# Performance work log

Measured on AMD Instinct MI355X. Metric: run time of the kernel, lower is better.

The kernel has to match this reference:

```python
import jax, jax.numpy as jnp
import numpy as np

EPS = 1e-6
BASE_CURVATURE = 1.0


def _artanh(x):
    return jnp.arctanh(jnp.clip(x, -1.0 + 1e-5, 1.0 - 1e-5))


def _norm(x):
    return jnp.maximum(jnp.linalg.norm(x, axis=-1, keepdims=True), EPS)


def _logmap0(x, c):
    # Poincare-ball log map at origin
    sc = jnp.sqrt(c)
    n = _norm(x)
    return _artanh(sc * n) * x / (sc * n)


def _expmap0(v, c):
    # Poincare-ball exp map at origin
    sc = jnp.sqrt(c)
    n = _norm(v)
    return jnp.tanh(sc * n) * v / (sc * n)


def _mobius_add(x, y, c):
    x2 = jnp.sum(x * x, axis=-1, keepdims=True)
    y2 = jnp.sum(y * y, axis=-1, keepdims=True)
    xy = jnp.sum(x * y, axis=-1, keepdims=True)
    num = (1.0 + 2.0 * c * xy + c * y2) * x + (1.0 - c * x2) * y
    den = 1.0 + 2.0 * c * xy + (c * c) * x2 * y2
    return num / jnp.maximum(den, EPS)


def _mobius_scalar_mul(t, x, c):
    sc = jnp.sqrt(c)
    n = _norm(x)
    return jnp.tanh(t * _artanh(sc * n)) * x / (sc * n)


def setup_inputs() -> dict:
    key = jax.random.key(0)
    ks = jax.random.split(key, 8)
    B, D_in, D_out, K = 4096, 2048, 2048, 4
    scale_w = np.sqrt(2.0 / (D_in + D_out)) * 0.1
    return {
        "x": jax.random.normal(ks[0], (B, D_in), jnp.float32) * 0.05,
        "weight": jax.random.normal(ks[1], (D_out, D_in), jnp.float32) * scale_w,
        "bias": jax.random.normal(ks[2], (D_out,), jnp.float32) * 0.01,
        "curv_weight": jax.random.normal(ks[3], (1, D_in), jnp.float32) * 0.1,
        "curv_bias": jnp.zeros((1,), jnp.float32),
        "anchors": jax.random.normal(ks[4], (K, D_out), jnp.float32) * 0.3,
        "t_values": jnp.full((K,), 0.5, jnp.float32),
        "anchor_weights": jnp.full((K,), 1.0 / K, jnp.float32),
    }


def reference(x, weight, bias, curv_weight, curv_bias, anchors, t_values, anchor_weights):
    # 1) dynamic curvature prediction: c_i = base_c * softplus(x . w + b), then mean
    logits = x @ curv_weight[0] + curv_bias[0]                 # [B]
    curvatures = BASE_CURVATURE * jax.nn.softplus(logits)      # [B]
    c = jax.lax.stop_gradient(jnp.mean(curvatures))            # scalar (.item() in torch)

    # 2) fused hyperbolic linear: expmap0(logmap0(x) @ W^T + b)
    u = _logmap0(x, c)                                         # [B, D_in]
    h = u @ weight.T + bias                                    # [B, D_out]
    y = _expmap0(h, c)                                         # [B, D_out]

    # 3) geodesic activation: weighted Mobius geodesic toward each anchor
    xe = y[:, None, :]                                         # [B, 1, D]
    a = anchors[None, :, :]                                    # [1, K, D]
    diff = _mobius_add(-xe, a, c)                              # [B, K, D]
    step = _mobius_scalar_mul(t_values[None, :, None], diff, c)
    g = _mobius_add(xe, step, c)                               # [B, K, D]
    w = jax.nn.softmax(anchor_weights)                         # [K]
    return jnp.einsum("bkd,k->bd", g, w)                       # [B, D_out]
```

## Files before the change

kernel.cpp:

```cpp
#include <hip/hip_runtime.h>
#include <stdint.h>

#define B_ROWS 4096
#define D_IN   2048
#define D_OUT  2048
#define KANCH  4

typedef _Float16 half8  __attribute__((ext_vector_type(8)));
typedef _Float16 half4  __attribute__((ext_vector_type(4)));
typedef float    floatx4 __attribute__((ext_vector_type(4)));
typedef const __attribute__((address_space(1))) uint8_t* gptr_t;
typedef __attribute__((address_space(3))) uint8_t* lptr_t;

__device__ __forceinline__ float frcp(float x)   { return __builtin_amdgcn_rcpf(x); }
__device__ __forceinline__ float ftanh(float x)  { float e = __expf(2.f * x); return (e - 1.f) * frcp(e + 1.f); }
__device__ __forceinline__ float fatanh(float z) { return 0.5f * __logf((1.f + z) * frcp(1.f - z)); }

__global__ __launch_bounds__(256) void k_prep(
    const float* __restrict__ x,
    const float* __restrict__ W,
    const float* __restrict__ cw,
    const float* __restrict__ cb,
    const float* __restrict__ bias,
    const float* __restrict__ anchors,
    _Float16* __restrict__ xh,
    _Float16* __restrict__ Wh,
    float* __restrict__ n2x,
    float* __restrict__ spart,
    float* __restrict__ scal)
{
    int tid = threadIdx.x;
    if (blockIdx.x < 1024) {
        int w = tid >> 6, lane = tid & 63;
        int row = blockIdx.x * 4 + w;
        const floatx4* xr = (const floatx4*)(x + (size_t)row * D_IN);
        const floatx4* wr = (const floatx4*)cw;
        _Float16* xo = xh + (size_t)row * D_IN;
        float dot = 0.f, ss = 0.f;
#pragma unroll
        for (int i = 0; i < 8; ++i) {
            int idx = i * 64 + lane;
            floatx4 xv = xr[idx];
            floatx4 wv = wr[idx];
#pragma unroll
            for (int j = 0; j < 4; ++j) {
                dot += xv[j] * wv[j];
                ss  += xv[j] * xv[j];
            }
            half4 h = {(_Float16)xv[0], (_Float16)xv[1], (_Float16)xv[2], (_Float16)xv[3]};
            *(half4*)(xo + idx * 4) = h;
        }
#pragma unroll
        for (int off = 32; off; off >>= 1) {
            dot += __shfl_down(dot, off);
            ss  += __shfl_down(ss, off);
        }
        __shared__ float spw[4];
        if (lane == 0) {
            n2x[row] = ss;
            float z = dot + cb[0];
            spw[w] = (z > 20.f) ? z : log1pf(expf(z));
        }
        __syncthreads();
        if (tid == 0)
            spart[blockIdx.x] = spw[0] + spw[1] + spw[2] + spw[3];
    } else if (blockIdx.x < 2048) {
        int blk = blockIdx.x - 1024;
        const floatx4* W4 = (const floatx4*)W;
#pragma unroll
        for (int i = 0; i < 4; ++i) {
            int idx = blk * 1024 + i * 256 + tid;
            floatx4 v = W4[idx];
            half4 h = {(_Float16)v[0], (_Float16)v[1], (_Float16)v[2], (_Float16)v[3]};
            *(half4*)(Wh + (size_t)idx * 4) = h;
        }
    } else {
        int w = tid >> 6, lane = tid & 63;
        float bf[8], af[KANCH][8];
        *(floatx4*)(bf)     = *(const floatx4*)(bias + tid * 8);
        *(floatx4*)(bf + 4) = *(const floatx4*)(bias + tid * 8 + 4);
#pragma unroll
        for (int k = 0; k < KANCH; ++k) {
            *(floatx4*)(af[k])     = *(const floatx4*)(anchors + (size_t)k * D_OUT + tid * 8);
            *(floatx4*)(af[k] + 4) = *(const floatx4*)(anchors + (size_t)k * D_OUT + tid * 8 + 4);
        }
        float v[9];
#pragma unroll
        for (int q = 0; q < 9; ++q) v[q] = 0.f;
#pragma unroll
        for (int j = 0; j < 8; ++j) {
            v[0] += bf[j] * bf[j];
#pragma unroll
            for (int k = 0; k < KANCH; ++k) {
                v[1 + k] += bf[j] * af[k][j];
                v[5 + k] += af[k][j] * af[k][j];
            }
        }
#pragma unroll
        for (int off = 32; off; off >>= 1)
#pragma unroll
            for (int q = 0; q < 9; ++q) v[q] += __shfl_down(v[q], off);
        __shared__ float red[4][9];
        if (lane == 0)
#pragma unroll
            for (int q = 0; q < 9; ++q) red[w][q] = v[q];
        __syncthreads();
        if (tid == 0)
#pragma unroll
            for (int q = 0; q < 9; ++q)
                scal[1 + q] = red[0][q] + red[1][q] + red[2][q] + red[3][q];
    }
}

template<int KPB>
__global__ __launch_bounds__(512, 2) void k_gemm(
    const _Float16* __restrict__ A,
    const _Float16* __restrict__ W,
    _Float16* __restrict__ P0,
    _Float16* __restrict__ P1)
{
    constexpr int NT = KPB / 64;
    __shared__ __align__(16) _Float16 lds[2][2][2][8192];
    const int tid  = threadIdx.x;
    const int lane = tid & 63;
    const int w    = tid >> 6;
    const int wm   = w >> 2;
    const int wn   = w & 3;
    const int bm0  = blockIdx.y * 256;
    const int bn0  = blockIdx.x * 256;
    const int kbase = blockIdx.z * KPB;
    _Float16* P = (blockIdx.z == 0) ? P0 : P1;

    const int e0 = tid * 16;
    const int srow = w * 16 + (lane & 15);
    const int scol = (lane >> 4) * 8;
    const size_t asrc = (size_t)(bm0 + srow) * D_IN + scol + kbase;
    const size_t bsrc = (size_t)(bn0 + srow) * D_IN + scol + kbase;
    const int wmoff = wm * 8192;
    const int wnoff = wn * 4096;
    const int loff  = lane * 16;

#define STAGE_Q(OP, D, KH, GP, SRC, KB) do { \
    uint8_t* qb_ = (uint8_t*)&lds[OP][D][KH][0]; \
    __builtin_amdgcn_global_load_lds((gptr_t)((GP) + (SRC) + (KB)), (lptr_t)(qb_ + e0), 16, 0, 0); \
    __builtin_amdgcn_global_load_lds((gptr_t)((GP) + (SRC) + (size_t)128 * D_IN + (KB)), (lptr_t)(qb_ + e0 + 8192), 16, 0, 0); \
} while (0)

    floatx4 acc[8][4];
#pragma unroll
    for (int mi = 0; mi < 8; ++mi)
#pragma unroll
        for (int ni = 0; ni < 4; ++ni)
            acc[mi][ni] = (floatx4){0.f, 0.f, 0.f, 0.f};

    STAGE_Q(0, 0, 0, A, asrc, 0);
    STAGE_Q(0, 0, 1, A, asrc, 32);
    STAGE_Q(1, 0, 0, W, bsrc, 0);
    STAGE_Q(1, 0, 1, W, bsrc, 32);
    STAGE_Q(0, 1, 0, A, asrc, 64);
    STAGE_Q(1, 1, 0, W, bsrc, 64);
    STAGE_Q(1, 1, 1, W, bsrc, 96);
    asm volatile("s_waitcnt vmcnt(6)" ::: "memory");
    __builtin_amdgcn_s_barrier();
    __builtin_amdgcn_sched_barrier(0);

    half8 aq[4], bq[4];

#define LOAD_A4(D, KH, MI0) do { _Pragma("unroll") \
    for (int mi = 0; mi < 4; ++mi) \
        aq[mi] = *(const half8*)((const uint8_t*)&lds[0][D][KH][0] + wmoff + ((MI0) + mi) * 1024 + loff); \
} while (0)
#define LOAD_B4(D, KH) do { _Pragma("unroll") \
    for (int ni = 0; ni < 4; ++ni) \
        bq[ni] = *(const half8*)((const uint8_t*)&lds[1][D][KH][0] + wnoff + ni * 1024 + loff); \
} while (0)
#define MFMA16(MI0) do { \
    __builtin_amdgcn_s_barrier(); \
    asm volatile("s_waitcnt lgkmcnt(0)" ::: "memory"); \
    __builtin_amdgcn_sched_barrier(0); \
    __builtin_amdgcn_s_setprio(1); \
    _Pragma("unroll") for (int mi = 0; mi < 4; ++mi) \
    _Pragma("unroll") for (int ni = 0; ni < 4; ++ni) \
        acc[(MI0) + mi][ni] = __builtin_amdgcn_mfma_f32_16x16x32_f16(aq[mi], bq[ni], acc[(MI0) + mi][ni], 0, 0, 0); \
    __builtin_amdgcn_s_setprio(0); \
    __builtin_amdgcn_sched_barrier(0); \
} while (0)
#define ENDPH() do { __builtin_amdgcn_s_barrier(); __builtin_amdgcn_sched_barrier(0); } while (0)

#define TILE_BODY(T, D) do { \
    LOAD_A4(D, 0, 0); LOAD_B4(D, 0); \
    if ((T) + 1 < NT) STAGE_Q(0, (D) ^ 1, 1, A, asrc, ((T) + 1) * 64 + 32); \
    MFMA16(0); ENDPH(); \
    LOAD_A4(D, 0, 4); \
    if ((T) + 2 < NT) STAGE_Q(1, D, 0, W, bsrc, ((T) + 2) * 64); \
    MFMA16(4); ENDPH(); \
    LOAD_A4(D, 1, 0); LOAD_B4(D, 1); \
    if ((T) + 2 < NT) STAGE_Q(0, D, 0, A, asrc, ((T) + 2) * 64); \
    MFMA16(0); ENDPH(); \
    LOAD_A4(D, 1, 4); \
    if ((T) + 2 < NT) STAGE_Q(1, D, 1, W, bsrc, ((T) + 2) * 64 + 32); \
    MFMA16(4); \
    if ((T) < NT - 2) asm volatile("s_waitcnt vmcnt(6)" ::: "memory"); \
    else              asm volatile("s_waitcnt vmcnt(0)" ::: "memory"); \
    ENDPH(); \
} while (0)

    for (int t = 0; t < NT; t += 2) {
        TILE_BODY(t, 0);
        TILE_BODY(t + 1, 1);
    }

#undef TILE_BODY
#undef ENDPH
#undef MFMA16
#undef LOAD_B4
#undef LOAD_A4
#undef STAGE_Q

#pragma unroll
    for (int mi = 0; mi < 8; ++mi) {
#pragma unroll
        for (int r = 0; r < 4; ++r) {
            int gm = bm0 + wm * 128 + mi * 16 + (lane >> 4) * 4 + r;
#pragma unroll
            for (int ni = 0; ni < 4; ++ni) {
                int gn = bn0 + wn * 64 + ni * 16 + (lane & 15);
                P[(size_t)gm * D_OUT + gn] = (_Float16)acc[mi][ni][r];
            }
        }
    }
}

__global__ __launch_bounds__(256) void k_mobius(
    const _Float16* __restrict__ P0,
    const _Float16* __restrict__ P1,
    const float* __restrict__ bias,
    const float* __restrict__ anchors,
    const float* __restrict__ tv,
    const float* __restrict__ aw,
    const float* __restrict__ n2x,
    const float* __restrict__ spart,
    const float* __restrict__ scal,
    int split,
    float* __restrict__ out)
{
    int tid = threadIdx.x, w = tid >> 6, lane = tid & 63;
    size_t rowoff = (size_t)blockIdx.x * D_OUT;
    float pf[8], bf[8];
    {
        half8 p = *(const half8*)(P0 + rowoff + tid * 8);
#pragma unroll
        for (int j = 0; j < 8; ++j) pf[j] = (float)p[j];
    }
    if (split == 2) {
        half8 q = *(const half8*)(P1 + rowoff + tid * 8);
#pragma unroll
        for (int j = 0; j < 8; ++j) pf[j] += (float)q[j];
    }
    *(floatx4*)(bf)     = *(const floatx4*)(bias + tid * 8);
    *(floatx4*)(bf + 4) = *(const floatx4*)(bias + tid * 8 + 4);
    float af[KANCH][8];
#pragma unroll
    for (int k = 0; k < KANCH; ++k) {
        *(floatx4*)(af[k])     = *(const floatx4*)(anchors + (size_t)k * D_OUT + tid * 8);
        *(floatx4*)(af[k] + 4) = *(const floatx4*)(anchors + (size_t)k * D_OUT + tid * 8 + 4);
    }
    float v[7];
#pragma unroll
    for (int q = 0; q < 7; ++q) v[q] = 0.f;
    {
        floatx4 s4 = ((const floatx4*)spart)[tid];
        v[6] = s4[0] + s4[1] + s4[2] + s4[3];
    }
#pragma unroll
    for (int j = 0; j < 8; ++j) {
        v[0] += pf[j] * pf[j];
        v[1] += pf[j] * bf[j];
#pragma unroll
        for (int k = 0; k < KANCH; ++k) v[2 + k] += pf[j] * af[k][j];
    }
#pragma unroll
    for (int off = 32; off; off >>= 1)
#pragma unroll
        for (int q = 0; q < 7; ++q) v[q] += __shfl_down(v[q], off);
    __shared__ float red[4][7];
    __shared__ float cf[2 + KANCH];
    if (lane == 0)
#pragma unroll
        for (int q = 0; q < 7; ++q) red[w][q] = v[q];
    __syncthreads();
    if (w == 0) {
        int k = lane & 3;
        float pp = red[0][0] + red[1][0] + red[2][0] + red[3][0];
        float pb = red[0][1] + red[1][1] + red[2][1] + red[3][1];
        float pa = red[0][2 + k] + red[1][2 + k] + red[2][2 + k] + red[3][2 + k];
        float spsum = red[0][6] + red[1][6] + red[2][6] + red[3][6];
        float bb = scal[1];
        float ba = scal[2 + k];
        float aa = scal[6 + k];
        float c = spsum * (1.0f / (float)B_ROWS);
        float sc = __builtin_amdgcn_sqrtf(c);
        float nx = fmaxf(__builtin_amdgcn_sqrtf(n2x[blockIdx.x]), 1e-6f);
        float ax = sc * nx;
        float zx = fminf(fmaxf(ax, -1.f + 1e-5f), 1.f - 1e-5f);
        float f = fatanh(zx) * frcp(ax);
        float hh = f * f * pp + 2.f * f * pb + bb;
        float ha = f * pa + ba;
        float ek = __expf(aw[k]);
        float se = ek;
        se += __shfl_xor(se, 1);
        se += __shfl_xor(se, 2);
        float wk = ek * frcp(se);
        float nh = fmaxf(__builtin_amdgcn_sqrtf(hh), 1e-6f);
        float snh = sc * nh;
        float gy = ftanh(snh) * frcp(snh);
        float x2 = gy * gy * hh;
        float B1 = 1.f - c * x2;
        float y2 = aa;
        float dy = gy * ha;
        float A1 = 1.f - 2.f * c * dy + c * y2;
        float den1 = fmaxf(1.f - 2.f * c * dy + c * c * x2 * y2, 1e-6f);
        float rd1 = frcp(den1);
        float al = -A1 * rd1, be = B1 * rd1;
        float nd2 = fmaxf(al * al * x2 + 2.f * al * be * dy + be * be * y2, 0.f);
        float nd = fmaxf(__builtin_amdgcn_sqrtf(nd2), 1e-6f);
        float snd = sc * nd;
        float zc = fminf(fmaxf(snd, -1.f + 1e-5f), 1.f - 1e-5f);
        float s = ftanh(tv[k] * fatanh(zc)) * frcp(snd);
        float y2s = s * s * nd2;
        float xys = s * (al * x2 + be * dy);
        float A2 = 1.f + 2.f * c * xys + c * y2s;
        float den2 = fmaxf(1.f + 2.f * c * xys + c * c * x2 * y2s, 1e-6f);
        float rd2 = frcp(den2);
        float Cy  = (A2 + B1 * s * al) * rd2;
        float Cak = (B1 * s * be) * rd2;
        float chk = wk * Cy;
        chk += __shfl_xor(chk, 1);
        chk += __shfl_xor(chk, 2);
        if (lane == 0) {
            float c0 = gy * chk;
            cf[0] = c0 * f;
            cf[1] = c0;
        }
        if (lane < 4) cf[2 + lane] = wk * Cak;
    }
    __syncthreads();
    float cp = cf[0], cb_ = cf[1];
    float o[8];
#pragma unroll
    for (int j = 0; j < 8; ++j) {
        float val = cp * pf[j] + cb_ * bf[j];
#pragma unroll
        for (int k = 0; k < KANCH; ++k) val += cf[2 + k] * af[k][j];
        o[j] = val;
    }
    *(floatx4*)(out + rowoff + tid * 8)     = *(floatx4*)(o);
    *(floatx4*)(out + rowoff + tid * 8 + 4) = *(floatx4*)(o + 4);
}

extern "C" void kernel_launch(void* const* d_in, const int* in_sizes, int n_in,
                              void* d_out, int out_size, void* d_ws, size_t ws_size,
                              hipStream_t stream) {
    const float* x       = (const float*)d_in[0];
    const float* wt      = (const float*)d_in[1];
    const float* bias    = (const float*)d_in[2];
    const float* cw      = (const float*)d_in[3];
    const float* cb      = (const float*)d_in[4];
    const float* anchors = (const float*)d_in[5];
    const float* tv      = (const float*)d_in[6];
    const float* aw      = (const float*)d_in[7];
    float* out = (float*)d_out;

    _Float16* Wh = (_Float16*)d_ws;
    _Float16* xh = Wh + (size_t)D_OUT * D_IN;
    float* n2x   = (float*)(xh + (size_t)B_ROWS * D_IN);
    float* spart = n2x + B_ROWS;
    float* scal  = spart + 1024;
    _Float16* P0 = (_Float16*)(scal + 16);
    _Float16* P1 = P0 + (size_t)B_ROWS * D_OUT;
    size_t need2 = (size_t)((char*)(P1 + (size_t)B_ROWS * D_OUT) - (char*)d_ws);
    int split = (ws_size >= need2) ? 2 : 1;

    k_prep<<<2049, 256, 0, stream>>>(x, wt, cw, cb, bias, anchors, xh, Wh, n2x, spart, scal);
    if (split == 2)
        k_gemm<D_IN / 2><<<dim3(D_OUT / 256, B_ROWS / 256, 2), 512, 0, stream>>>(xh, Wh, P0, P1);
    else
        k_gemm<D_IN><<<dim3(D_OUT / 256, B_ROWS / 256, 1), 512, 0, stream>>>(xh, Wh, P0, P1);
    k_mobius<<<B_ROWS, 256, 0, stream>>>(P0, P1, bias, anchors, tv, aw, n2x, spart, scal, split, out);
}
```

Measured before the change: 162.3 us.

## Remap GEMM tiles per XCD, relax sched barriers, batch rows in mobius

The GEMM block index is remapped so each of the 8 XCDs works on a compact group of M/N tiles (and a single K-split half), which should improve L2 reuse of A and W inside each XCD. The sched_barrier and explicit lgkmcnt waits around the MFMA phases are removed, so the compiler handles LDS-load/MFMA ordering. The mobius kernel now processes 8 rows per block, loading bias/anchors and computing curvature/softmax once per block instead of once per row. Removing the explicit waits leaves synchronization of LDS reads to the compiler's inserted waitcnts, and fewer mobius blocks lowers parallelism.

```diff
diff --git a/kernel.cpp b/kernel.cpp
--- a/kernel.cpp
+++ b/kernel.cpp
@@ -5,6 +5,7 @@
 #define D_IN   2048
 #define D_OUT  2048
 #define KANCH  4
+#define MROWS  8
 
 typedef _Float16 half8  __attribute__((ext_vector_type(8)));
 typedef _Float16 half4  __attribute__((ext_vector_type(4)));
@@ -120,16 +121,32 @@
     _Float16* __restrict__ P1)
 {
     constexpr int NT = KPB / 64;
+    constexpr int NZ = (KPB == D_IN) ? 1 : 2;
     __shared__ __align__(16) _Float16 lds[2][2][2][8192];
     const int tid  = threadIdx.x;
     const int lane = tid & 63;
     const int w    = tid >> 6;
     const int wm   = w >> 2;
     const int wn   = w & 3;
-    const int bm0  = blockIdx.y * 256;
-    const int bn0  = blockIdx.x * 256;
-    const int kbase = blockIdx.z * KPB;
-    _Float16* P = (blockIdx.z == 0) ? P0 : P1;
+
+    int lin = (blockIdx.z * gridDim.y + blockIdx.y) * gridDim.x + blockIdx.x;
+    int xcd = lin & 7;
+    int i   = lin >> 3;
+    int zz, mt, nt;
+    if (NZ == 2) {
+        zz = xcd & 1;
+        int grp = xcd >> 1;
+        mt = (grp >> 1) * 8 + (i >> 2);
+        nt = (grp & 1) * 4 + (i & 3);
+    } else {
+        zz = 0;
+        mt = (xcd >> 1) * 4 + (i >> 2);
+        nt = (xcd & 1) * 4 + (i & 3);
+    }
+    const int bm0 = mt * 256;
+    const int bn0 = nt * 256;
+    const int kbase = zz * KPB;
+    _Float16* P = (zz == 0) ? P0 : P1;
 
     const int e0 = tid * 16;
     const int srow = w * 16 + (lane & 15);
@@ -162,7 +179,6 @@
     STAGE_Q(1, 1, 1, W, bsrc, 96);
     asm volatile("s_waitcnt vmcnt(6)" ::: "memory");
     __builtin_amdgcn_s_barrier();
-    __builtin_amdgcn_sched_barrier(0);
 
     half8 aq[4], bq[4];
 
@@ -176,16 +192,13 @@
 } while (0)
 #define MFMA16(MI0) do { \
     __builtin_amdgcn_s_barrier(); \
-    asm volatile("s_waitcnt lgkmcnt(0)" ::: "memory"); \
-    __builtin_amdgcn_sched_barrier(0); \
     __builtin_amdgcn_s_setprio(1); \
     _Pragma("unroll") for (int mi = 0; mi < 4; ++mi) \
     _Pragma("unroll") for (int ni = 0; ni < 4; ++ni) \
         acc[(MI0) + mi][ni] = __builtin_amdgcn_mfma_f32_16x16x32_f16(aq[mi], bq[ni], acc[(MI0) + mi][ni], 0, 0, 0); \
     __builtin_amdgcn_s_setprio(0); \
-    __builtin_amdgcn_sched_barrier(0); \
 } while (0)
-#define ENDPH() do { __builtin_amdgcn_s_barrier(); __builtin_amdgcn_sched_barrier(0); } while (0)
+#define ENDPH() __builtin_amdgcn_s_barrier()
 
 #define TILE_BODY(T, D) do { \
     LOAD_A4(D, 0, 0); LOAD_B4(D, 0); \
@@ -245,18 +258,7 @@
     float* __restrict__ out)
 {
     int tid = threadIdx.x, w = tid >> 6, lane = tid & 63;
-    size_t rowoff = (size_t)blockIdx.x * D_OUT;
-    float pf[8], bf[8];
-    {
-        half8 p = *(const half8*)(P0 + rowoff + tid * 8);
-#pragma unroll
-        for (int j = 0; j < 8; ++j) pf[j] = (float)p[j];
-    }
-    if (split == 2) {
-        half8 q = *(const half8*)(P1 + rowoff + tid * 8);
-#pragma unroll
-        for (int j = 0; j < 8; ++j) pf[j] += (float)q[j];
-    }
+    float bf[8];
     *(floatx4*)(bf)     = *(const floatx4*)(bias + tid * 8);
     *(floatx4*)(bf + 4) = *(const floatx4*)(bias + tid * 8 + 4);
     float af[KANCH][8];
@@ -265,97 +267,124 @@
         *(floatx4*)(af[k])     = *(const floatx4*)(anchors + (size_t)k * D_OUT + tid * 8);
         *(floatx4*)(af[k] + 4) = *(const floatx4*)(anchors + (size_t)k * D_OUT + tid * 8 + 4);
     }
-    float v[7];
-#pragma unroll
-    for (int q = 0; q < 7; ++q) v[q] = 0.f;
+    float v6;
     {
         floatx4 s4 = ((const floatx4*)spart)[tid];
-        v[6] = s4[0] + s4[1] + s4[2] + s4[3];
-    }
-#pragma unroll
-    for (int j = 0; j < 8; ++j) {
-        v[0] += pf[j] * pf[j];
-        v[1] += pf[j] * bf[j];
-#pragma unroll
-        for (int k = 0; k < KANCH; ++k) v[2 + k] += pf[j] * af[k][j];
-    }
-#pragma unroll
-    for (int off = 32; off; off >>= 1)
-#pragma unroll
-        for (int q = 0; q < 7; ++q) v[q] += __shfl_down(v[q], off);
-    __shared__ float red[4][7];
+        v6 = s4[0] + s4[1] + s4[2] + s4[3];
+    }
+#pragma unroll
+    for (int off = 32; off; off >>= 1) v6 += __shfl_down(v6, off);
+    __shared__ float redS[4];
+    __shared__ float red[4][6];
     __shared__ float cf[2 + KANCH];
-    if (lane == 0)
-#pragma unroll
-        for (int q = 0; q < 7; ++q) red[w][q] = v[q];
+    if (lane == 0) redS[w] = v6;
     __syncthreads();
+
+    int k = lane & 3;
+    float c = 0.f, sc = 0.f, wk = 0.f, tvk = 0.f, bb = 0.f, ba = 0.f, aa = 0.f;
     if (w == 0) {
-        int k = lane & 3;
-        float pp = red[0][0] + red[1][0] + red[2][0] + red[3][0];
-        float pb = red[0][1] + red[1][1] + red[2][1] + red[3][1];
-        float pa = red[0][2 + k] + red[1][2 + k] + red[2][2 + k] + red[3][2 + k];
-        float spsum = red[0][6] + red[1][6] + red[2][6] + red[3][6];
-        float bb = scal[1];
-        float ba = scal[2 + k];
-        float aa = scal[6 + k];
-        float c = spsum * (1.0f / (float)B_ROWS);
-        float sc = __builtin_amdgcn_sqrtf(c);
-        float nx = fmaxf(__builtin_amdgcn_sqrtf(n2x[blockIdx.x]), 1e-6f);
-        float ax = sc * nx;
-        float zx = fminf(fmaxf(ax, -1.f + 1e-5f), 1.f - 1e-5f);
-        float f = fatanh(zx) * frcp(ax);
-        float hh = f * f * pp + 2.f * f * pb + bb;
-        float ha = f * pa + ba;
+        float spsum = redS[0] + redS[1] + redS[2] + redS[3];
+        c  = spsum * (1.0f / (float)B_ROWS);
+        sc = __builtin_amdgcn_sqrtf(c);
         float ek = __expf(aw[k]);
         float se = ek;
         se += __shfl_xor(se, 1);
         se += __shfl_xor(se, 2);
-        float wk = ek * frcp(se);
-        float nh = fmaxf(__builtin_amdgcn_sqrtf(hh), 1e-6f);
-        float snh = sc * nh;
-        float gy = ftanh(snh) * frcp(snh);
-        float x2 = gy * gy * hh;
-        float B1 = 1.f - c * x2;
-        float y2 = aa;
-        float dy = gy * ha;
-        float A1 = 1.f - 2.f * c * dy + c * y2;
-        float den1 = fmaxf(1.f - 2.f * c * dy + c * c * x2 * y2, 1e-6f);
-        float rd1 = frcp(den1);
-        float al = -A1 * rd1, be = B1 * rd1;
-        float nd2 = fmaxf(al * al * x2 + 2.f * al * be * dy + be * be * y2, 0.f);
-        float nd = fmaxf(__builtin_amdgcn_sqrtf(nd2), 1e-6f);
-        float snd = sc * nd;
-        float zc = fminf(fmaxf(snd, -1.f + 1e-5f), 1.f - 1e-5f);
-        float s = ftanh(tv[k] * fatanh(zc)) * frcp(snd);
-        float y2s = s * s * nd2;
-        float xys = s * (al * x2 + be * dy);
-        float A2 = 1.f + 2.f * c * xys + c * y2s;
-        float den2 = fmaxf(1.f + 2.f * c * xys + c * c * x2 * y2s, 1e-6f);
-        float rd2 = frcp(den2);
-        float Cy  = (A2 + B1 * s * al) * rd2;
-        float Cak = (B1 * s * be) * rd2;
-        float chk = wk * Cy;
-        chk += __shfl_xor(chk, 1);
-        chk += __shfl_xor(chk, 2);
-        if (lane == 0) {
-            float c0 = gy * chk;
-            cf[0] = c0 * f;
-            cf[1] = c0;
-        }
-        if (lane < 4) cf[2 + lane] = wk * Cak;
-    }
-    __syncthreads();
-    float cp = cf[0], cb_ = cf[1];
-    float o[8];
-#pragma unroll
-    for (int j = 0; j < 8; ++j) {
-        float val = cp * pf[j] + cb_ * bf[j];
-#pragma unroll
-        for (int k = 0; k < KANCH; ++k) val += cf[2 + k] * af[k][j];
-        o[j] = val;
-    }
-    *(floatx4*)(out + rowoff + tid * 8)     = *(floatx4*)(o);
-    *(floatx4*)(out + rowoff + tid * 8 + 4) = *(floatx4*)(o + 4);
+        wk = ek * frcp(se);
+        tvk = tv[k];
+        bb = scal[1];
+        ba = scal[2 + k];
+        aa = scal[6 + k];
+    }
+
+    for (int r = 0; r < MROWS; ++r) {
+        int row = blockIdx.x * MROWS + r;
+        size_t rowoff = (size_t)row * D_OUT;
+        float pf[8];
+        {
+            half8 p = *(const half8*)(P0 + rowoff + tid * 8);
+#pragma unroll
+            for (int j = 0; j < 8; ++j) pf[j] = (float)p[j];
+        }
+        if (split == 2) {
+            half8 q = *(const half8*)(P1 + rowoff + tid * 8);
+#pragma unroll
+            for (int j = 0; j < 8; ++j) pf[j] += (float)q[j];
+        }
+        float v[6];
+#pragma unroll
+        for (int q = 0; q < 6; ++q) v[q] = 0.f;
+#pragma unroll
+        for (int j = 0; j < 8; ++j) {
+            v[0] += pf[j] * pf[j];
+            v[1] += pf[j] * bf[j];
+#pragma unroll
+            for (int kk = 0; kk < KANCH; ++kk) v[2 + kk] += pf[j] * af[kk][j];
+        }
+#pragma unroll
+        for (int off = 32; off; off >>= 1)
+#pragma unroll
+            for (int q = 0; q < 6; ++q) v[q] += __shfl_down(v[q], off);
+        if (lane == 0)
+#pragma unroll
+            for (int q = 0; q < 6; ++q) red[w][q] = v[q];
+        __syncthreads();
+        if (w == 0) {
+            float pp = red[0][0] + red[1][0] + red[2][0] + red[3][0];
+            float pb = red[0][1] + red[1][1] + red[2][1] + red[3][1];
+            float pa = red[0][2 + k] + red[1][2 + k] + red[2][2 + k] + red[3][2 + k];
+            float nx = fmaxf(__builtin_amdgcn_sqrtf(n2x[row]), 1e-6f);
+            float ax = sc * nx;
+            float zx = fminf(fmaxf(ax, -1.f + 1e-5f), 1.f - 1e-5f);
+            float f = fatanh(zx) * frcp(ax);
+            float hh = f * f * pp + 2.f * f * pb + bb;
+            float ha = f * pa + ba;
+            float nh = fmaxf(__builtin_amdgcn_sqrtf(hh), 1e-6f);
+            float snh = sc * nh;
+            float gy = ftanh(snh) * frcp(snh);
+            float x2 = gy * gy * hh;
+            float B1 = 1.f - c * x2;
+            float y2 = aa;
+            float dy = gy * ha;
+            float A1 = 1.f - 2.f * c * dy + c * y2;
+            float den1 = fmaxf(1.f - 2.f * c * dy + c * c * x2 * y2, 1e-6f);
+            float rd1 = frcp(den1);
+            float al = -A1 * rd1, be = B1 * rd1;
+            float nd2 = fmaxf(al * al * x2 + 2.f * al * be * dy + be * be * y2, 0.f);
+            float nd = fmaxf(__builtin_amdgcn_sqrtf(nd2), 1e-6f);
+            float snd = sc * nd;
+            float zc = fminf(fmaxf(snd, -1.f + 1e-5f), 1.f - 1e-5f);
+            float s = ftanh(tvk * fatanh(zc)) * frcp(snd);
+            float y2s = s * s * nd2;
+            float xys = s * (al * x2 + be * dy);
+            float A2 = 1.f + 2.f * c * xys + c * y2s;
+            float den2 = fmaxf(1.f + 2.f * c * xys + c * c * x2 * y2s, 1e-6f);
+            float rd2 = frcp(den2);
+            float Cy  = (A2 + B1 * s * al) * rd2;
+            float Cak = (B1 * s * be) * rd2;
+            float chk = wk * Cy;
+            chk += __shfl_xor(chk, 1);
+            chk += __shfl_xor(chk, 2);
+            if (lane == 0) {
+                float c0 = gy * chk;
+                cf[0] = c0 * f;
+                cf[1] = c0;
+            }
+            if (lane < 4) cf[2 + lane] = wk * Cak;
+        }
+        __syncthreads();
+        float cp = cf[0], cb_ = cf[1];
+        float o[8];
+#pragma unroll
+        for (int j = 0; j < 8; ++j) {
+            float val = cp * pf[j] + cb_ * bf[j];
+#pragma unroll
+            for (int kk = 0; kk < KANCH; ++kk) val += cf[2 + kk] * af[kk][j];
+            o[j] = val;
+        }
+        *(floatx4*)(out + rowoff + tid * 8)     = *(floatx4*)(o);
+        *(floatx4*)(out + rowoff + tid * 8 + 4) = *(floatx4*)(o + 4);
+    }
 }
 
 extern "C" void kernel_launch(void* const* d_in, const int* in_sizes, int n_in,
@@ -383,8 +412,8 @@
 
     k_prep<<<2049, 256, 0, stream>>>(x, wt, cw, cb, bias, anchors, xh, Wh, n2x, spart, scal);
     if (split == 2)
-        k_gemm<D_IN / 2><<<dim3(D_OUT / 256, B_ROWS / 256, 2), 512, 0, stream>>>(xh, Wh, P0, P1);
+        k_gemm<D_IN / 2><<<dim3(8, 16, 2), 512, 0, stream>>>(xh, Wh, P0, P1);
     else
-        k_gemm<D_IN><<<dim3(D_OUT / 256, B_ROWS / 256, 1), 512, 0, stream>>>(xh, Wh, P0, P1);
-    k_mobius<<<B_ROWS, 256, 0, stream>>>(P0, P1, bias, anchors, tv, aw, n2x, spart, scal, split, out);
+        k_gemm<D_IN><<<dim3(8, 16, 1), 512, 0, stream>>>(xh, Wh, P0, P1);
+    k_mobius<<<B_ROWS / MROWS, 256, 0, stream>>>(P0, P1, bias, anchors, tv, aw, n2x, spart, scal, split, out);
 }
```

Result: slower. 168.6 us (+3.9%).

## Remap GEMM blocks per XCD and double-buffer LDS fragment loads across phases

Applied to the files above, without the earlier changes.

Replaces the hardware block order with an XCD-aware mapping, so blocks on the same XCD share M/N tiles and the K-split half, which should improve L2 reuse. Restructures the inner tile loop so the LDS fragment reads for the next MFMA phase are issued before the barrier and current phase's MFMAs. It uses separate even and odd register sets for this. The explicit lgkmcnt(0) waits and sched_barriers are dropped and the compiler now inserts the waits. This raises register pressure and relies on the barrier placement to avoid races between LDS reads and async global-to-LDS staging into the same buffers.

```diff
diff --git a/kernel.cpp b/kernel.cpp
--- a/kernel.cpp
+++ b/kernel.cpp
@@ -120,16 +120,32 @@
     _Float16* __restrict__ P1)
 {
     constexpr int NT = KPB / 64;
+    constexpr int NZ = (KPB == D_IN) ? 1 : 2;
     __shared__ __align__(16) _Float16 lds[2][2][2][8192];
     const int tid  = threadIdx.x;
     const int lane = tid & 63;
     const int w    = tid >> 6;
     const int wm   = w >> 2;
     const int wn   = w & 3;
-    const int bm0  = blockIdx.y * 256;
-    const int bn0  = blockIdx.x * 256;
-    const int kbase = blockIdx.z * KPB;
-    _Float16* P = (blockIdx.z == 0) ? P0 : P1;
+
+    int lin = (blockIdx.z * gridDim.y + blockIdx.y) * gridDim.x + blockIdx.x;
+    int xcd = lin & 7;
+    int i   = lin >> 3;
+    int zz, mt, nt;
+    if (NZ == 2) {
+        zz = xcd & 1;
+        int grp = xcd >> 1;
+        mt = (grp >> 1) * 8 + (i >> 2);
+        nt = (grp & 1) * 4 + (i & 3);
+    } else {
+        zz = 0;
+        mt = (xcd >> 1) * 4 + (i >> 2);
+        nt = (xcd & 1) * 4 + (i & 3);
+    }
+    const int bm0 = mt * 256;
+    const int bn0 = nt * 256;
+    const int kbase = zz * KPB;
+    _Float16* P = (zz == 0) ? P0 : P1;
 
     const int e0 = tid * 16;
     const int srow = w * 16 + (lane & 15);
@@ -162,47 +178,49 @@
     STAGE_Q(1, 1, 1, W, bsrc, 96);
     asm volatile("s_waitcnt vmcnt(6)" ::: "memory");
     __builtin_amdgcn_s_barrier();
-    __builtin_amdgcn_sched_barrier(0);
-
-    half8 aq[4], bq[4];
-
-#define LOAD_A4(D, KH, MI0) do { _Pragma("unroll") \
+
+    half8 aqE[4], bqE[4], aqO[4], bqO[4];
+
+#define LOAD_A4(AQ, D, KH, MI0) do { _Pragma("unroll") \
     for (int mi = 0; mi < 4; ++mi) \
-        aq[mi] = *(const half8*)((const uint8_t*)&lds[0][D][KH][0] + wmoff + ((MI0) + mi) * 1024 + loff); \
+        AQ[mi] = *(const half8*)((const uint8_t*)&lds[0][D][KH][0] + wmoff + ((MI0) + mi) * 1024 + loff); \
 } while (0)
-#define LOAD_B4(D, KH) do { _Pragma("unroll") \
+#define LOAD_B4(BQ, D, KH) do { _Pragma("unroll") \
     for (int ni = 0; ni < 4; ++ni) \
-        bq[ni] = *(const half8*)((const uint8_t*)&lds[1][D][KH][0] + wnoff + ni * 1024 + loff); \
+        BQ[ni] = *(const half8*)((const uint8_t*)&lds[1][D][KH][0] + wnoff + ni * 1024 + loff); \
 } while (0)
-#define MFMA16(MI0) do { \
-    __builtin_amdgcn_s_barrier(); \
-    asm volatile("s_waitcnt lgkmcnt(0)" ::: "memory"); \
-    __builtin_amdgcn_sched_barrier(0); \
+#define MFMA_Q(AQ, BQ, MI0) do { \
     __builtin_amdgcn_s_setprio(1); \
     _Pragma("unroll") for (int mi = 0; mi < 4; ++mi) \
     _Pragma("unroll") for (int ni = 0; ni < 4; ++ni) \
-        acc[(MI0) + mi][ni] = __builtin_amdgcn_mfma_f32_16x16x32_f16(aq[mi], bq[ni], acc[(MI0) + mi][ni], 0, 0, 0); \
+        acc[(MI0) + mi][ni] = __builtin_amdgcn_mfma_f32_16x16x32_f16(AQ[mi], BQ[ni], acc[(MI0) + mi][ni], 0, 0, 0); \
     __builtin_amdgcn_s_setprio(0); \
-    __builtin_amdgcn_sched_barrier(0); \
 } while (0)
-#define ENDPH() do { __builtin_amdgcn_s_barrier(); __builtin_amdgcn_sched_barrier(0); } while (0)
+#define PH_BAR() __builtin_amdgcn_s_barrier()
 
 #define TILE_BODY(T, D) do { \
-    LOAD_A4(D, 0, 0); LOAD_B4(D, 0); \
+     \
+    LOAD_A4(aqE, D, 0, 0); LOAD_B4(bqE, D, 0); LOAD_A4(aqO, D, 0, 4); \
     if ((T) + 1 < NT) STAGE_Q(0, (D) ^ 1, 1, A, asrc, ((T) + 1) * 64 + 32); \
-    MFMA16(0); ENDPH(); \
-    LOAD_A4(D, 0, 4); \
+    PH_BAR(); \
+    MFMA_Q(aqE, bqE, 0); \
+     \
+    LOAD_A4(aqE, D, 1, 0); LOAD_B4(bqO, D, 1); \
     if ((T) + 2 < NT) STAGE_Q(1, D, 0, W, bsrc, ((T) + 2) * 64); \
-    MFMA16(4); ENDPH(); \
-    LOAD_A4(D, 1, 0); LOAD_B4(D, 1); \
+    PH_BAR(); \
+    MFMA_Q(aqO, bqE, 4); \
+     \
+    LOAD_A4(aqO, D, 1, 4); \
     if ((T) + 2 < NT) STAGE_Q(0, D, 0, A, asrc, ((T) + 2) * 64); \
-    MFMA16(0); ENDPH(); \
-    LOAD_A4(D, 1, 4); \
+    PH_BAR(); \
+    MFMA_Q(aqE, bqO, 0); \
+     \
     if ((T) + 2 < NT) STAGE_Q(1, D, 1, W, bsrc, ((T) + 2) * 64 + 32); \
-    MFMA16(4); \
+    PH_BAR(); \
+    MFMA_Q(aqO, bqO, 4); \
     if ((T) < NT - 2) asm volatile("s_waitcnt vmcnt(6)" ::: "memory"); \
     else              asm volatile("s_waitcnt vmcnt(0)" ::: "memory"); \
-    ENDPH(); \
+    PH_BAR(); \
 } while (0)
 
     for (int t = 0; t < NT; t += 2) {
@@ -211,8 +229,8 @@
     }
 
 #undef TILE_BODY
-#undef ENDPH
-#undef MFMA16
+#undef PH_BAR
+#undef MFMA_Q
 #undef LOAD_B4
 #undef LOAD_A4
 #undef STAGE_Q
@@ -383,8 +401,8 @@
 
     k_prep<<<2049, 256, 0, stream>>>(x, wt, cw, cb, bias, anchors, xh, Wh, n2x, spart, scal);
     if (split == 2)
-        k_gemm<D_IN / 2><<<dim3(D_OUT / 256, B_ROWS / 256, 2), 512, 0, stream>>>(xh, Wh, P0, P1);
+        k_gemm<D_IN / 2><<<dim3(8, 16, 2), 512, 0, stream>>>(xh, Wh, P0, P1);
     else
-        k_gemm<D_IN><<<dim3(D_OUT / 256, B_ROWS / 256, 1), 512, 0, stream>>>(xh, Wh, P0, P1);
+        k_gemm<D_IN><<<dim3(8, 16, 1), 512, 0, stream>>>(xh, Wh, P0, P1);
     k_mobius<<<B_ROWS, 256, 0, stream>>>(P0, P1, bias, anchors, tv, aw, n2x, spart, scal, split, out);
 }
```

Measured after the change: 162.5 us. About the same (+0.1%).
